# Optimization experiments

Hardware: AMD Instinct MI355X
Metric: run time of the kernel (lower is better)

## Reference

```python
import jax, jax.numpy as jnp
import numpy as np

N = 1_000_000
FEAT_DIM = 256
N_CLASS = 345
N_DOMAIN = 6
BETA = 0.5
EPS = 1e-5


def setup_inputs() -> dict:
    key = jax.random.key(0)
    k1, k2, k3, k4 = jax.random.split(key, 4)
    feats = jax.random.normal(k1, (N, FEAT_DIM), dtype=jnp.float32)
    mean = jax.random.normal(k2, (N_DOMAIN, N_CLASS, FEAT_DIM), dtype=jnp.float32)
    amount = jnp.zeros((N_DOMAIN, N_CLASS), dtype=jnp.float32)
    labels = jax.random.randint(k3, (N,), 0, N_CLASS, dtype=jnp.int64 if jax.config.jax_enable_x64 else jnp.int32)
    domains = jax.random.randint(k4, (N,), 0, N_DOMAIN, dtype=jnp.int64 if jax.config.jax_enable_x64 else jnp.int32)
    return {"feats": feats, "mean": mean, "amount": amount,
            "labels": labels, "domains": domains}


def reference(feats, mean, amount, labels, domains):
    # Segmented per-(domain, class) mean of feats. Equivalent to the original
    # onehot broadcast-multiply + sum, but without the O(N*C*F) intermediate.
    seg = domains * N_CLASS + labels  # [N]
    sums = jax.ops.segment_sum(feats, seg, num_segments=N_DOMAIN * N_CLASS)
    sums = sums.reshape(N_DOMAIN, N_CLASS, FEAT_DIM)
    counts = jax.ops.segment_sum(jnp.ones((feats.shape[0],), dtype=feats.dtype), seg,
                                 num_segments=N_DOMAIN * N_CLASS)
    counts = counts.reshape(N_DOMAIN, N_CLASS)

    tmp_mean = sums / (counts[..., None] + EPS)  # [D, C, F]
    # Mask of (domain, class) cells actually observed (tmp_mean row nonzero)
    tmp_mask = (jnp.sum(tmp_mean, axis=-1) != 0).astype(feats.dtype)[..., None]  # [D, C, 1]

    new_mean = mean * (1.0 - tmp_mask) + (mean * BETA + tmp_mean * (1.0 - BETA)) * tmp_mask
    new_amount = jnp.where(counts > 0, jnp.ones_like(amount), amount)
    return new_mean, new_amount
```

## Files before the change

### kernel.cpp

```cpp
#include <hip/hip_runtime.h>
#include <stddef.h>

constexpr int FEAT = 256;
constexpr int F4   = FEAT / 4;
constexpr int NCLS = 345;
constexpr int NDOM = 6;
constexpr int NSEG = NCLS * NDOM;
constexpr int SB   = 256;
constexpr float BETA = 0.5f;
constexpr float EPS  = 1e-5f;

typedef float f32x4 __attribute__((ext_vector_type(4)));

__global__ void __launch_bounds__(256)
k_seg_hist(const int* __restrict__ labels, const int* __restrict__ domains,
           int n, int chunk, int* __restrict__ seg, int* __restrict__ W) {
    __shared__ int h[NSEG];
    for (int i = threadIdx.x; i < NSEG; i += blockDim.x) h[i] = 0;
    __syncthreads();
    const int b  = blockIdx.x;
    const int lo = b * chunk;
    const int hi = min(n, lo + chunk);
    for (int i = lo + threadIdx.x; i < hi; i += blockDim.x) {
        int s = domains[i] * NCLS + labels[i];
        seg[i] = s;
        atomicAdd(&h[s], 1);
    }
    __syncthreads();
    int* Wb = W + (size_t)b * NSEG;
    for (int i = threadIdx.x; i < NSEG; i += blockDim.x) Wb[i] = h[i];
}

__global__ void __launch_bounds__(256)
k_bases_tot(const int* __restrict__ W, int* __restrict__ Bmat,
            int* __restrict__ totals) {
    const int s = blockIdx.x;
    const int t = threadIdx.x;
    __shared__ int sc[SB];
    int w = W[(size_t)t * NSEG + s];
    sc[t] = w;
    __syncthreads();
    for (int off = 1; off < SB; off <<= 1) {
        int v = (t >= off) ? sc[t - off] : 0;
        __syncthreads();
        sc[t] += v;
        __syncthreads();
    }
    Bmat[(size_t)t * NSEG + s] = sc[t] - w;
    if (t == SB - 1) totals[s] = sc[t];
}

__global__ void k_scan(const int* __restrict__ totals, int* __restrict__ offsets) {
    constexpr int T  = 256;
    constexpr int CH = (NSEG + T - 1) / T;
    __shared__ int csum[T];
    int t = threadIdx.x;
    int base = t * CH;
    int sum = 0;
    for (int j = 0; j < CH; ++j) {
        int idx = base + j;
        if (idx < NSEG) sum += totals[idx];
    }
    csum[t] = sum;
    __syncthreads();
    for (int off = 1; off < T; off <<= 1) {
        int v = (t >= off) ? csum[t - off] : 0;
        __syncthreads();
        csum[t] += v;
        __syncthreads();
    }
    int run = csum[t] - sum;
    for (int j = 0; j < CH; ++j) {
        int idx = base + j;
        if (idx < NSEG) {
            offsets[idx] = run;
            run += totals[idx];
        }
    }
}

__global__ void __launch_bounds__(256)
k_scatter(const int* __restrict__ seg, int n, int chunk,
          const int* __restrict__ Bmat, const int* __restrict__ offsets,
          int* __restrict__ sorted) {
    __shared__ int cur[NSEG];
    const int b = blockIdx.x;
    const int* Bb = Bmat + (size_t)b * NSEG;
    for (int i = threadIdx.x; i < NSEG; i += blockDim.x) cur[i] = Bb[i] + offsets[i];
    __syncthreads();
    const int lo = b * chunk;
    const int hi = min(n, lo + chunk);
    for (int i = lo + threadIdx.x; i < hi; i += blockDim.x) {
        int s = seg[i];
        int pos = atomicAdd(&cur[s], 1);
        sorted[pos] = i;
    }
}

__global__ void __launch_bounds__(256)
k_reduce(const float* __restrict__ feats, const float* __restrict__ mean,
         const float* __restrict__ amount, const int* __restrict__ sorted,
         const int* __restrict__ counts, const int* __restrict__ offsets,
         float* __restrict__ out) {
    const int seg  = blockIdx.x;
    const int cnt  = counts[seg];
    const int base = offsets[seg];
    const int lane = threadIdx.x & 63;
    const int rp   = threadIdx.x >> 6;

    f32x4 acc = (f32x4)0.0f;
    int r = rp;
    for (; r + 28 < cnt; r += 32) {
        int i0 = sorted[base + r];
        int i1 = sorted[base + r + 4];
        int i2 = sorted[base + r + 8];
        int i3 = sorted[base + r + 12];
        int i4 = sorted[base + r + 16];
        int i5 = sorted[base + r + 20];
        int i6 = sorted[base + r + 24];
        int i7 = sorted[base + r + 28];
        f32x4 v0 = reinterpret_cast<const f32x4*>(feats + (size_t)i0 * FEAT)[lane];
        f32x4 v1 = reinterpret_cast<const f32x4*>(feats + (size_t)i1 * FEAT)[lane];
        f32x4 v2 = reinterpret_cast<const f32x4*>(feats + (size_t)i2 * FEAT)[lane];
        f32x4 v3 = reinterpret_cast<const f32x4*>(feats + (size_t)i3 * FEAT)[lane];
        f32x4 v4 = reinterpret_cast<const f32x4*>(feats + (size_t)i4 * FEAT)[lane];
        f32x4 v5 = reinterpret_cast<const f32x4*>(feats + (size_t)i5 * FEAT)[lane];
        f32x4 v6 = reinterpret_cast<const f32x4*>(feats + (size_t)i6 * FEAT)[lane];
        f32x4 v7 = reinterpret_cast<const f32x4*>(feats + (size_t)i7 * FEAT)[lane];
        acc += (v0 + v1) + (v2 + v3) + ((v4 + v5) + (v6 + v7));
    }
    for (; r < cnt; r += 4) {
        int i0 = sorted[base + r];
        acc += reinterpret_cast<const f32x4*>(feats + (size_t)i0 * FEAT)[lane];
    }

    __shared__ f32x4 sh[4][F4];
    sh[rp][lane] = acc;
    __syncthreads();
    if (rp == 0) {
        f32x4 s = acc + sh[1][lane] + sh[2][lane] + sh[3][lane];
        float inv = 1.0f / ((float)cnt + EPS);
        f32x4 tm = s * inv;

        float lsum = tm.x + tm.y + tm.z + tm.w;
        for (int off = 1; off < 64; off <<= 1) lsum += __shfl_xor(lsum, off, 64);
        bool msk = (lsum != 0.0f);

        f32x4 m4 = reinterpret_cast<const f32x4*>(mean)[(size_t)seg * F4 + lane];
        f32x4 o = msk ? (m4 * BETA + tm * (1.0f - BETA)) : m4;
        reinterpret_cast<f32x4*>(out)[(size_t)seg * F4 + lane] = o;
        if (lane == 0) {
            out[(size_t)NSEG * FEAT + seg] = (cnt > 0) ? 1.0f : amount[seg];
        }
    }
}

__global__ void k_fb_zero(float* __restrict__ out, int total) {
    int stride = gridDim.x * blockDim.x;
    for (int i = blockIdx.x * blockDim.x + threadIdx.x; i < total; i += stride) out[i] = 0.f;
}

__global__ void k_fb_acc(const float* __restrict__ feats, const int* __restrict__ labels,
                         const int* __restrict__ domains, int n, float* __restrict__ out) {
    int lane   = threadIdx.x & 63;
    int gwave  = (blockIdx.x * blockDim.x + threadIdx.x) >> 6;
    int nwaves = (gridDim.x * blockDim.x) >> 6;
    for (int i = gwave; i < n; i += nwaves) {
        int seg = domains[i] * NCLS + labels[i];
        const float4 v = reinterpret_cast<const float4*>(feats + (size_t)i * FEAT)[lane];
        float* dst = out + (size_t)seg * FEAT + lane * 4;
        atomicAdd(dst + 0, v.x);
        atomicAdd(dst + 1, v.y);
        atomicAdd(dst + 2, v.z);
        atomicAdd(dst + 3, v.w);
        if (lane == 0) atomicAdd(out + (size_t)NSEG * FEAT + seg, 1.0f);
    }
}

__global__ void k_fb_epi(const float* __restrict__ mean, const float* __restrict__ amount,
                         float* __restrict__ out) {
    int seg  = blockIdx.x;
    int lane = threadIdx.x;
    float cntf = out[(size_t)NSEG * FEAT + seg];
    float4 s = reinterpret_cast<float4*>(out)[(size_t)seg * F4 + lane];
    float inv = 1.0f / (cntf + EPS);
    float4 tm = make_float4(s.x * inv, s.y * inv, s.z * inv, s.w * inv);
    float lsum = tm.x + tm.y + tm.z + tm.w;
    for (int off = 1; off < 64; off <<= 1) lsum += __shfl_xor(lsum, off, 64);
    bool msk = (lsum != 0.0f);
    float4 m4 = reinterpret_cast<const float4*>(mean)[(size_t)seg * F4 + lane];
    float4 o;
    if (msk) {
        o.x = m4.x * BETA + tm.x * (1.f - BETA);
        o.y = m4.y * BETA + tm.y * (1.f - BETA);
        o.z = m4.z * BETA + tm.z * (1.f - BETA);
        o.w = m4.w * BETA + tm.w * (1.f - BETA);
    } else {
        o = m4;
    }
    reinterpret_cast<float4*>(out)[(size_t)seg * F4 + lane] = o;
    if (lane == 0) {
        out[(size_t)NSEG * FEAT + seg] = (cntf > 0.5f) ? 1.0f : amount[seg];
    }
}

extern "C" void kernel_launch(void* const* d_in, const int* in_sizes, int n_in,
                              void* d_out, int out_size, void* d_ws, size_t ws_size,
                              hipStream_t stream) {
    const float* feats   = (const float*)d_in[0];
    const float* mean    = (const float*)d_in[1];
    const float* amount  = (const float*)d_in[2];
    const int*   labels  = (const int*)d_in[3];
    const int*   domains = (const int*)d_in[4];
    float* out = (float*)d_out;
    const int n = in_sizes[3];
    const int chunk = (n + SB - 1) / SB;

    size_t need = ((size_t)n * 2 + (size_t)SB * NSEG * 2 + (size_t)NSEG * 2) * sizeof(int);
    if (ws_size >= need) {
        int* seg     = (int*)d_ws;
        int* W       = seg + n;
        int* totals  = W + (size_t)SB * NSEG;
        int* offsets = totals + NSEG;
        int* Bmat    = offsets + NSEG;
        int* sorted  = Bmat + (size_t)SB * NSEG;

        k_seg_hist<<<SB, 256, 0, stream>>>(labels, domains, n, chunk, seg, W);
        k_bases_tot<<<NSEG, 256, 0, stream>>>(W, Bmat, totals);
        k_scan<<<1, 256, 0, stream>>>(totals, offsets);
        k_scatter<<<SB, 256, 0, stream>>>(seg, n, chunk, Bmat, offsets, sorted);
        k_reduce<<<NSEG, 256, 0, stream>>>(feats, mean, amount, sorted, totals, offsets, out);
    } else {
        int total = NSEG * FEAT + NSEG;
        k_fb_zero<<<(total + 255) / 256, 256, 0, stream>>>(out, total);
        k_fb_acc<<<2048, 256, 0, stream>>>(feats, labels, domains, n, out);
        k_fb_epi<<<NSEG, 64, 0, stream>>>(mean, amount, out);
    }
}
```

Measured before the change: 237.3 us.

## Split per-segment reduction into four quarter blocks and fuse scan into scatter

```diff
diff --git a/kernel.cpp b/kernel.cpp
--- a/kernel.cpp
+++ b/kernel.cpp
@@ -7,6 +7,7 @@
 constexpr int NDOM = 6;
 constexpr int NSEG = NCLS * NDOM;
 constexpr int SB   = 256;
+constexpr int QS   = 4;
 constexpr float BETA = 0.5f;
 constexpr float EPS  = 1e-5f;
 
@@ -50,20 +51,28 @@
     if (t == SB - 1) totals[s] = sc[t];
 }
 
-__global__ void k_scan(const int* __restrict__ totals, int* __restrict__ offsets) {
-    constexpr int T  = 256;
-    constexpr int CH = (NSEG + T - 1) / T;
-    __shared__ int csum[T];
-    int t = threadIdx.x;
-    int base = t * CH;
+__global__ void __launch_bounds__(256)
+k_scatter(const int* __restrict__ seg, int n, int chunk,
+          const int* __restrict__ Bmat, const int* __restrict__ totals,
+          int* __restrict__ offsets, int* __restrict__ sorted) {
+    constexpr int CH = (NSEG + 255) / 256;
+    __shared__ int cur[NSEG];
+    __shared__ int toff[NSEG];
+    __shared__ int csum[256];
+    const int b = blockIdx.x;
+    const int t = threadIdx.x;
+
+    for (int i = t; i < NSEG; i += 256) toff[i] = totals[i];
+    __syncthreads();
+    const int cbase = t * CH;
     int sum = 0;
     for (int j = 0; j < CH; ++j) {
-        int idx = base + j;
-        if (idx < NSEG) sum += totals[idx];
+        int idx = cbase + j;
+        if (idx < NSEG) sum += toff[idx];
     }
     csum[t] = sum;
     __syncthreads();
-    for (int off = 1; off < T; off <<= 1) {
+    for (int off = 1; off < 256; off <<= 1) {
         int v = (t >= off) ? csum[t - off] : 0;
         __syncthreads();
         csum[t] += v;
@@ -71,26 +80,21 @@
     }
     int run = csum[t] - sum;
     for (int j = 0; j < CH; ++j) {
-        int idx = base + j;
-        if (idx < NSEG) {
-            offsets[idx] = run;
-            run += totals[idx];
-        }
-    }
-}
-
-__global__ void __launch_bounds__(256)
-k_scatter(const int* __restrict__ seg, int n, int chunk,
-          const int* __restrict__ Bmat, const int* __restrict__ offsets,
-          int* __restrict__ sorted) {
-    __shared__ int cur[NSEG];
-    const int b = blockIdx.x;
+        int idx = cbase + j;
+        if (idx < NSEG) { int v = toff[idx]; toff[idx] = run; run += v; }
+    }
+    __syncthreads();
+
     const int* Bb = Bmat + (size_t)b * NSEG;
-    for (int i = threadIdx.x; i < NSEG; i += blockDim.x) cur[i] = Bb[i] + offsets[i];
-    __syncthreads();
+    for (int i = t; i < NSEG; i += 256) {
+        cur[i] = Bb[i] + toff[i];
+        if (b == 0) offsets[i] = toff[i];
+    }
+    __syncthreads();
+
     const int lo = b * chunk;
     const int hi = min(n, lo + chunk);
-    for (int i = lo + threadIdx.x; i < hi; i += blockDim.x) {
+    for (int i = lo + t; i < hi; i += 256) {
         int s = seg[i];
         int pos = atomicAdd(&cur[s], 1);
         sorted[pos] = i;
@@ -98,27 +102,33 @@
 }
 
 __global__ void __launch_bounds__(256)
-k_reduce(const float* __restrict__ feats, const float* __restrict__ mean,
-         const float* __restrict__ amount, const int* __restrict__ sorted,
-         const int* __restrict__ counts, const int* __restrict__ offsets,
-         float* __restrict__ out) {
-    const int seg  = blockIdx.x;
-    const int cnt  = counts[seg];
-    const int base = offsets[seg];
+k_reduce4(const float* __restrict__ feats, const int* __restrict__ sorted,
+          const int* __restrict__ totals, const int* __restrict__ offsets,
+          float* __restrict__ partial) {
+    const int b   = blockIdx.x;
+    const int seg = b >> 2;
+    const int q   = b & 3;
+    const int cnt = totals[seg];
+    const int cq  = (cnt + QS - 1) >> 2;
+    const int lo  = min(cnt, q * cq);
+    const int hi  = min(cnt, lo + cq);
+    const int qn  = hi - lo;
+    const int qbase = offsets[seg] + lo;
+
     const int lane = threadIdx.x & 63;
     const int rp   = threadIdx.x >> 6;
 
     f32x4 acc = (f32x4)0.0f;
     int r = rp;
-    for (; r + 28 < cnt; r += 32) {
-        int i0 = sorted[base + r];
-        int i1 = sorted[base + r + 4];
-        int i2 = sorted[base + r + 8];
-        int i3 = sorted[base + r + 12];
-        int i4 = sorted[base + r + 16];
-        int i5 = sorted[base + r + 20];
-        int i6 = sorted[base + r + 24];
-        int i7 = sorted[base + r + 28];
+    for (; r + 28 < qn; r += 32) {
+        int i0 = sorted[qbase + r];
+        int i1 = sorted[qbase + r + 4];
+        int i2 = sorted[qbase + r + 8];
+        int i3 = sorted[qbase + r + 12];
+        int i4 = sorted[qbase + r + 16];
+        int i5 = sorted[qbase + r + 20];
+        int i6 = sorted[qbase + r + 24];
+        int i7 = sorted[qbase + r + 28];
         f32x4 v0 = reinterpret_cast<const f32x4*>(feats + (size_t)i0 * FEAT)[lane];
         f32x4 v1 = reinterpret_cast<const f32x4*>(feats + (size_t)i1 * FEAT)[lane];
         f32x4 v2 = reinterpret_cast<const f32x4*>(feats + (size_t)i2 * FEAT)[lane];
@@ -129,8 +139,8 @@
         f32x4 v7 = reinterpret_cast<const f32x4*>(feats + (size_t)i7 * FEAT)[lane];
         acc += (v0 + v1) + (v2 + v3) + ((v4 + v5) + (v6 + v7));
     }
-    for (; r < cnt; r += 4) {
-        int i0 = sorted[base + r];
+    for (; r < qn; r += 4) {
+        int i0 = sorted[qbase + r];
         acc += reinterpret_cast<const f32x4*>(feats + (size_t)i0 * FEAT)[lane];
     }
 
@@ -139,19 +149,33 @@
     __syncthreads();
     if (rp == 0) {
         f32x4 s = acc + sh[1][lane] + sh[2][lane] + sh[3][lane];
-        float inv = 1.0f / ((float)cnt + EPS);
-        f32x4 tm = s * inv;
-
-        float lsum = tm.x + tm.y + tm.z + tm.w;
-        for (int off = 1; off < 64; off <<= 1) lsum += __shfl_xor(lsum, off, 64);
-        bool msk = (lsum != 0.0f);
-
-        f32x4 m4 = reinterpret_cast<const f32x4*>(mean)[(size_t)seg * F4 + lane];
-        f32x4 o = msk ? (m4 * BETA + tm * (1.0f - BETA)) : m4;
-        reinterpret_cast<f32x4*>(out)[(size_t)seg * F4 + lane] = o;
-        if (lane == 0) {
-            out[(size_t)NSEG * FEAT + seg] = (cnt > 0) ? 1.0f : amount[seg];
-        }
+        reinterpret_cast<f32x4*>(partial)[(size_t)b * F4 + lane] = s;
+    }
+}
+
+__global__ void k_final(const float* __restrict__ partial, const float* __restrict__ mean,
+                        const float* __restrict__ amount, const int* __restrict__ totals,
+                        float* __restrict__ out) {
+    const int seg  = blockIdx.x;
+    const int lane = threadIdx.x;
+    const int cnt  = totals[seg];
+    const f32x4* P = reinterpret_cast<const f32x4*>(partial);
+    f32x4 s = P[(size_t)(4 * seg + 0) * F4 + lane]
+            + P[(size_t)(4 * seg + 1) * F4 + lane]
+            + P[(size_t)(4 * seg + 2) * F4 + lane]
+            + P[(size_t)(4 * seg + 3) * F4 + lane];
+    float inv = 1.0f / ((float)cnt + EPS);
+    f32x4 tm = s * inv;
+
+    float lsum = tm.x + tm.y + tm.z + tm.w;
+    for (int off = 1; off < 64; off <<= 1) lsum += __shfl_xor(lsum, off, 64);
+    bool msk = (lsum != 0.0f);
+
+    f32x4 m4 = reinterpret_cast<const f32x4*>(mean)[(size_t)seg * F4 + lane];
+    f32x4 o = msk ? (m4 * BETA + tm * (1.0f - BETA)) : m4;
+    reinterpret_cast<f32x4*>(out)[(size_t)seg * F4 + lane] = o;
+    if (lane == 0) {
+        out[(size_t)NSEG * FEAT + seg] = (cnt > 0) ? 1.0f : amount[seg];
     }
 }
 
@@ -216,20 +240,22 @@
     const int n = in_sizes[3];
     const int chunk = (n + SB - 1) / SB;
 
-    size_t need = ((size_t)n * 2 + (size_t)SB * NSEG * 2 + (size_t)NSEG * 2) * sizeof(int);
+    size_t need = ((size_t)n * 2 + (size_t)SB * NSEG * 2
+                   + (size_t)QS * NSEG * FEAT + (size_t)NSEG * 2) * sizeof(int);
     if (ws_size >= need) {
-        int* seg     = (int*)d_ws;
-        int* W       = seg + n;
-        int* totals  = W + (size_t)SB * NSEG;
-        int* offsets = totals + NSEG;
-        int* Bmat    = offsets + NSEG;
-        int* sorted  = Bmat + (size_t)SB * NSEG;
+        int*   seg     = (int*)d_ws;
+        int*   sorted  = seg + n;
+        int*   W       = sorted + n;
+        int*   Bmat    = W + (size_t)SB * NSEG;
+        float* partial = (float*)(Bmat + (size_t)SB * NSEG);
+        int*   totals  = (int*)(partial + (size_t)QS * NSEG * FEAT);
+        int*   offsets = totals + NSEG;
 
         k_seg_hist<<<SB, 256, 0, stream>>>(labels, domains, n, chunk, seg, W);
         k_bases_tot<<<NSEG, 256, 0, stream>>>(W, Bmat, totals);
-        k_scan<<<1, 256, 0, stream>>>(totals, offsets);
-        k_scatter<<<SB, 256, 0, stream>>>(seg, n, chunk, Bmat, offsets, sorted);
-        k_reduce<<<NSEG, 256, 0, stream>>>(feats, mean, amount, sorted, totals, offsets, out);
+        k_scatter<<<SB, 256, 0, stream>>>(seg, n, chunk, Bmat, totals, offsets, sorted);
+        k_reduce4<<<QS * NSEG, 256, 0, stream>>>(feats, sorted, totals, offsets, partial);
+        k_final<<<NSEG, 64, 0, stream>>>(partial, mean, amount, totals, out);
     } else {
         int total = NSEG * FEAT + NSEG;
         k_fb_zero<<<(total + 255) / 256, 256, 0, stream>>>(out, total);
```

After: 244.8 us. +3.2%, slower.

## Split the tail segments across four blocks and recompute segment ids in scatter

Applied to the files above, without the earlier changes.

```diff
diff --git a/kernel.cpp b/kernel.cpp
--- a/kernel.cpp
+++ b/kernel.cpp
@@ -7,14 +7,16 @@
 constexpr int NDOM = 6;
 constexpr int NSEG = NCLS * NDOM;
 constexpr int SB   = 256;
+constexpr int NTAIL = 22;
+constexpr int NFULL = NSEG - NTAIL;
 constexpr float BETA = 0.5f;
 constexpr float EPS  = 1e-5f;
 
 typedef float f32x4 __attribute__((ext_vector_type(4)));
 
 __global__ void __launch_bounds__(256)
-k_seg_hist(const int* __restrict__ labels, const int* __restrict__ domains,
-           int n, int chunk, int* __restrict__ seg, int* __restrict__ W) {
+k_hist(const int* __restrict__ labels, const int* __restrict__ domains,
+       int n, int chunk, int* __restrict__ W) {
     __shared__ int h[NSEG];
     for (int i = threadIdx.x; i < NSEG; i += blockDim.x) h[i] = 0;
     __syncthreads();
@@ -23,7 +25,6 @@
     const int hi = min(n, lo + chunk);
     for (int i = lo + threadIdx.x; i < hi; i += blockDim.x) {
         int s = domains[i] * NCLS + labels[i];
-        seg[i] = s;
         atomicAdd(&h[s], 1);
     }
     __syncthreads();
@@ -80,9 +81,9 @@
 }
 
 __global__ void __launch_bounds__(256)
-k_scatter(const int* __restrict__ seg, int n, int chunk,
-          const int* __restrict__ Bmat, const int* __restrict__ offsets,
-          int* __restrict__ sorted) {
+k_scatter(const int* __restrict__ labels, const int* __restrict__ domains,
+          int n, int chunk, const int* __restrict__ Bmat,
+          const int* __restrict__ offsets, int* __restrict__ sorted) {
     __shared__ int cur[NSEG];
     const int b = blockIdx.x;
     const int* Bb = Bmat + (size_t)b * NSEG;
@@ -91,26 +92,41 @@
     const int lo = b * chunk;
     const int hi = min(n, lo + chunk);
     for (int i = lo + threadIdx.x; i < hi; i += blockDim.x) {
-        int s = seg[i];
+        int s = domains[i] * NCLS + labels[i];
         int pos = atomicAdd(&cur[s], 1);
         sorted[pos] = i;
     }
 }
 
 __global__ void __launch_bounds__(256)
-k_reduce(const float* __restrict__ feats, const float* __restrict__ mean,
-         const float* __restrict__ amount, const int* __restrict__ sorted,
-         const int* __restrict__ counts, const int* __restrict__ offsets,
-         float* __restrict__ out) {
-    const int seg  = blockIdx.x;
-    const int cnt  = counts[seg];
-    const int base = offsets[seg];
+k_reduce_mixed(const float* __restrict__ feats, const float* __restrict__ mean,
+               const float* __restrict__ amount, const int* __restrict__ sorted,
+               const int* __restrict__ totals, const int* __restrict__ offsets,
+               float* __restrict__ partial, float* __restrict__ out) {
+    const int b = blockIdx.x;
+    int seg, lo, hi, pslot = 0;
+    if (b < NFULL) {
+        seg = b;
+        lo = 0;
+        hi = totals[seg];
+    } else {
+        const int j  = b - NFULL;
+        seg = NFULL + (j >> 2);
+        const int q  = j & 3;
+        const int cnt = totals[seg];
+        const int cq  = (cnt + 3) >> 2;
+        lo = min(cnt, q * cq);
+        hi = min(cnt, lo + cq);
+        pslot = j;
+    }
+    const int qn   = hi - lo;
+    const int base = offsets[seg] + lo;
     const int lane = threadIdx.x & 63;
     const int rp   = threadIdx.x >> 6;
 
     f32x4 acc = (f32x4)0.0f;
     int r = rp;
-    for (; r + 28 < cnt; r += 32) {
+    for (; r + 28 < qn; r += 32) {
         int i0 = sorted[base + r];
         int i1 = sorted[base + r + 4];
         int i2 = sorted[base + r + 8];
@@ -129,7 +145,7 @@
         f32x4 v7 = reinterpret_cast<const f32x4*>(feats + (size_t)i7 * FEAT)[lane];
         acc += (v0 + v1) + (v2 + v3) + ((v4 + v5) + (v6 + v7));
     }
-    for (; r < cnt; r += 4) {
+    for (; r < qn; r += 4) {
         int i0 = sorted[base + r];
         acc += reinterpret_cast<const f32x4*>(feats + (size_t)i0 * FEAT)[lane];
     }
@@ -139,19 +155,49 @@
     __syncthreads();
     if (rp == 0) {
         f32x4 s = acc + sh[1][lane] + sh[2][lane] + sh[3][lane];
-        float inv = 1.0f / ((float)cnt + EPS);
-        f32x4 tm = s * inv;
-
-        float lsum = tm.x + tm.y + tm.z + tm.w;
-        for (int off = 1; off < 64; off <<= 1) lsum += __shfl_xor(lsum, off, 64);
-        bool msk = (lsum != 0.0f);
-
-        f32x4 m4 = reinterpret_cast<const f32x4*>(mean)[(size_t)seg * F4 + lane];
-        f32x4 o = msk ? (m4 * BETA + tm * (1.0f - BETA)) : m4;
-        reinterpret_cast<f32x4*>(out)[(size_t)seg * F4 + lane] = o;
-        if (lane == 0) {
-            out[(size_t)NSEG * FEAT + seg] = (cnt > 0) ? 1.0f : amount[seg];
+        if (b < NFULL) {
+            const int cnt = hi;
+            float inv = 1.0f / ((float)cnt + EPS);
+            f32x4 tm = s * inv;
+            float lsum = tm.x + tm.y + tm.z + tm.w;
+            for (int off = 1; off < 64; off <<= 1) lsum += __shfl_xor(lsum, off, 64);
+            bool msk = (lsum != 0.0f);
+            f32x4 m4 = reinterpret_cast<const f32x4*>(mean)[(size_t)seg * F4 + lane];
+            f32x4 o = msk ? (m4 * BETA + tm * (1.0f - BETA)) : m4;
+            reinterpret_cast<f32x4*>(out)[(size_t)seg * F4 + lane] = o;
+            if (lane == 0) {
+                out[(size_t)NSEG * FEAT + seg] = (cnt > 0) ? 1.0f : amount[seg];
+            }
+        } else {
+            reinterpret_cast<f32x4*>(partial)[(size_t)pslot * F4 + lane] = s;
         }
+    }
+}
+
+__global__ void k_final_tail(const float* __restrict__ partial, const float* __restrict__ mean,
+                             const float* __restrict__ amount, const int* __restrict__ totals,
+                             float* __restrict__ out) {
+    const int ts   = blockIdx.x;
+    const int seg  = NFULL + ts;
+    const int lane = threadIdx.x;
+    const int cnt  = totals[seg];
+    const f32x4* P = reinterpret_cast<const f32x4*>(partial);
+    f32x4 s = P[(size_t)(4 * ts + 0) * F4 + lane]
+            + P[(size_t)(4 * ts + 1) * F4 + lane]
+            + P[(size_t)(4 * ts + 2) * F4 + lane]
+            + P[(size_t)(4 * ts + 3) * F4 + lane];
+    float inv = 1.0f / ((float)cnt + EPS);
+    f32x4 tm = s * inv;
+
+    float lsum = tm.x + tm.y + tm.z + tm.w;
+    for (int off = 1; off < 64; off <<= 1) lsum += __shfl_xor(lsum, off, 64);
+    bool msk = (lsum != 0.0f);
+
+    f32x4 m4 = reinterpret_cast<const f32x4*>(mean)[(size_t)seg * F4 + lane];
+    f32x4 o = msk ? (m4 * BETA + tm * (1.0f - BETA)) : m4;
+    reinterpret_cast<f32x4*>(out)[(size_t)seg * F4 + lane] = o;
+    if (lane == 0) {
+        out[(size_t)NSEG * FEAT + seg] = (cnt > 0) ? 1.0f : amount[seg];
     }
 }
 
@@ -216,20 +262,23 @@
     const int n = in_sizes[3];
     const int chunk = (n + SB - 1) / SB;
 
-    size_t need = ((size_t)n * 2 + (size_t)SB * NSEG * 2 + (size_t)NSEG * 2) * sizeof(int);
+    size_t need = ((size_t)n + (size_t)SB * NSEG * 2
+                   + (size_t)4 * NTAIL * FEAT + (size_t)NSEG * 2) * sizeof(int);
     if (ws_size >= need) {
-        int* seg     = (int*)d_ws;
-        int* W       = seg + n;
-        int* totals  = W + (size_t)SB * NSEG;
-        int* offsets = totals + NSEG;
-        int* Bmat    = offsets + NSEG;
-        int* sorted  = Bmat + (size_t)SB * NSEG;
-
-        k_seg_hist<<<SB, 256, 0, stream>>>(labels, domains, n, chunk, seg, W);
+        int*   sorted  = (int*)d_ws;
+        int*   W       = sorted + n;
+        int*   Bmat    = W + (size_t)SB * NSEG;
+        float* partial = (float*)(Bmat + (size_t)SB * NSEG);
+        int*   totals  = (int*)(partial + (size_t)4 * NTAIL * FEAT);
+        int*   offsets = totals + NSEG;
+
+        k_hist<<<SB, 256, 0, stream>>>(labels, domains, n, chunk, W);
         k_bases_tot<<<NSEG, 256, 0, stream>>>(W, Bmat, totals);
         k_scan<<<1, 256, 0, stream>>>(totals, offsets);
-        k_scatter<<<SB, 256, 0, stream>>>(seg, n, chunk, Bmat, offsets, sorted);
-        k_reduce<<<NSEG, 256, 0, stream>>>(feats, mean, amount, sorted, totals, offsets, out);
+        k_scatter<<<SB, 256, 0, stream>>>(labels, domains, n, chunk, Bmat, offsets, sorted);
+        k_reduce_mixed<<<NFULL + 4 * NTAIL, 256, 0, stream>>>(
+            feats, mean, amount, sorted, totals, offsets, partial, out);
+        k_final_tail<<<NTAIL, 64, 0, stream>>>(partial, mean, amount, totals, out);
     } else {
         int total = NSEG * FEAT + NSEG;
         k_fb_zero<<<(total + 255) / 256, 256, 0, stream>>>(out, total);
```

After: 236.0 us, median of 2. About the same (-0.6%).
